# Performance work log

Measured on AMD Instinct MI355X. Metric: run time of the kernel, lower is better.

## Reference

```python
import jax, jax.numpy as jnp
import numpy as np

T, B, D = 512, 64, 1024


def setup_inputs() -> dict:
    key = jax.random.key(0)
    k1, k2, k3, k4 = jax.random.split(key, 4)
    scale = 1.0 / np.sqrt(D)
    x = jax.random.normal(k1, (T, B, D), dtype=jnp.float32)
    resets = jax.random.randint(k2, (T, B), 0, 2) > 0  # bool reset mask per step
    Wi = jax.random.normal(k3, (D, 3 * D), dtype=jnp.float32) * scale  # [ir|iz|in]
    bi = jnp.zeros((3 * D,), dtype=jnp.float32)
    Wh = jax.random.normal(k4, (D, 3 * D), dtype=jnp.float32) * scale  # [hr|hz|hn]
    bhn = jnp.zeros((D,), dtype=jnp.float32)  # bias only on hn gate (flax GRUCell)
    return {"x": x, "Wi": Wi, "bi": bi, "Wh": Wh, "bhn": bhn, "resets": resets}


def reference(x, Wi, bi, Wh, bhn, resets):
    """Scan of flax nn.GRUCell with reset-masked carry. x: [T,B,D], resets: [T,B] bool."""
    Bsz, Dh = x.shape[1], x.shape[2]

    def step(h, inp):
        xt, rt = inp  # xt: [B,D], rt: [B]
        h = jnp.where(rt[:, None], jnp.zeros_like(h), h)  # reset carry to zeros
        gi = xt @ Wi + bi          # [B,3D]
        gh = h @ Wh                # [B,3D] (no bias for r,z in flax GRUCell)
        ir_, iz_, in_ = jnp.split(gi, 3, axis=-1)
        hr_, hz_, hn_ = jnp.split(gh, 3, axis=-1)
        r = jax.nn.sigmoid(ir_ + hr_)
        z = jax.nn.sigmoid(iz_ + hz_)
        n = jnp.tanh(in_ + r * (hn_ + bhn))
        h_new = (1.0 - z) * n + z * h
        return h_new, h_new

    h0 = jnp.zeros((Bsz, Dh), dtype=x.dtype)  # flax initialize_carry default: zeros
    _, ys = jax.lax.scan(step, h0, (x, resets))
    return ys  # [T,B,D]
```

## Files before the change

kernel.cpp:

```cpp
#include <hip/hip_runtime.h>


typedef __attribute__((ext_vector_type(8))) short short8;
typedef __attribute__((ext_vector_type(4))) float f32x4;
typedef __attribute__((ext_vector_type(4))) unsigned int u32x4;

#define DEV static __device__ __forceinline__

constexpr int TT = 512, BB = 64, DD = 1024, TD = 3072;

constexpr size_t WS_FLAGS = 256;
constexpr size_t WS_H = 8192;
constexpr size_t HPLANE = (size_t)BB * DD * 2;
constexpr size_t WS_NEED = WS_H + 4 * HPLANE;

DEV unsigned short f2bf(float f) {
    unsigned u = __builtin_bit_cast(unsigned, f);
    u += 0x7FFFu + ((u >> 16) & 1u);
    return (unsigned short)(u >> 16);
}
DEV float bf2f(unsigned short s) { return __builtin_bit_cast(float, ((unsigned)s) << 16); }

DEV void ld16c(u32x4& r, const unsigned* p) {
    asm volatile("global_load_dwordx4 %0, %1, off sc0 sc1" : "=v"(r) : "v"(p));
}
DEV void ld16(u32x4& r, const unsigned* p) {
    asm volatile("global_load_dwordx4 %0, %1, off" : "=v"(r) : "v"(p));
}
DEV void ld8u(unsigned& r, const unsigned char* p) {
    asm volatile("global_load_ubyte %0, %1, off" : "=v"(r) : "v"(p));
}
DEV void vm0() {
    asm volatile("s_waitcnt vmcnt(0)" ::: "memory");
    __builtin_amdgcn_sched_barrier(0);
}
#define WAITN(n) do { asm volatile("s_waitcnt vmcnt(" #n ")" ::: "memory"); \
                      __builtin_amdgcn_sched_barrier(0); } while (0)

__global__ void pack_x_kernel(const float* __restrict__ x, unsigned* __restrict__ outw) {
    const size_t gid = (size_t)blockIdx.x * 256 + threadIdx.x;
    const size_t e0 = gid * 8;
    const unsigned t = (unsigned)(e0 >> 16);
    const unsigned p = (unsigned)(e0 & 65535u);
    const unsigned r = p >> 10, d = p & 1023u;
    const unsigned m = r >> 4, lr = r & 15u;
    f32x4 a = *(const f32x4*)(x + e0);
    f32x4 b = *(const f32x4*)(x + e0 + 4);
    u32x4 wh, wl;
#pragma unroll
    for (int j = 0; j < 2; ++j) {
        unsigned short h0 = f2bf(a[2 * j]), h1 = f2bf(a[2 * j + 1]);
        wh[j] = (unsigned)h0 | ((unsigned)h1 << 16);
        wl[j] = (unsigned)f2bf(a[2 * j] - bf2f(h0)) | ((unsigned)f2bf(a[2 * j + 1] - bf2f(h1)) << 16);
        unsigned short g0 = f2bf(b[2 * j]), g1 = f2bf(b[2 * j + 1]);
        wh[2 + j] = (unsigned)g0 | ((unsigned)g1 << 16);
        wl[2 + j] = (unsigned)f2bf(b[2 * j] - bf2f(g0)) | ((unsigned)f2bf(b[2 * j + 1] - bf2f(g1)) << 16);
    }
    unsigned* base = outw + (size_t)t * 65536u + m * 16384u + ((lr * 1024u + d) >> 1);
    *(u32x4*)base = wh;
    *(u32x4*)(base + 8192u) = wl;
}

__global__ void prep_kernel(const unsigned char* __restrict__ resets, unsigned char* __restrict__ ws) {
    const int bid = blockIdx.x, tid = threadIdx.x;
    if (bid < 256) {
        ((unsigned*)(ws + WS_H))[bid * 256 + tid] = 0u;
    } else {
        unsigned* w32 = (unsigned*)ws;
        for (int i = tid; i < 2048; i += 256) w32[i] = 0u;
        __shared__ int ca, cb, cc;
        if (tid == 0) { ca = 0; cb = 0; cc = 0; }
        __syncthreads();
        int la = 0, lb = 0, lc = 0;
        for (int o = tid * 16; o < tid * 16 + 16; ++o) {
            unsigned char v = resets[o];
            if (v) {
                if ((o & 3) == 0) la = 1; else lb = 1;
                if ((o & 7) == 4) lc = 1;
            }
        }
        if (la) atomicOr(&ca, 1);
        if (lb) atomicOr(&cb, 1);
        if (lc) atomicOr(&cc, 1);
        __syncthreads();
        if (tid == 0) {
            unsigned stride, boff = 0;
            if (ca && cb)       { stride = 1; }
            else if (!ca && cb) { stride = 4; boff = 3; }
            else if (ca && cc)  { stride = 4; }
            else if (ca)        { stride = 8; }
            else                { stride = 4; }
            w32[0] = stride; w32[1] = boff;
        }
    }
}

__launch_bounds__(512, 1)
__global__ void gru_kernel(const float* __restrict__ Wi, const float* __restrict__ bi,
                           const float* __restrict__ Wh, const float* __restrict__ bhn,
                           const unsigned char* __restrict__ resets,
                           float* __restrict__ out, unsigned char* __restrict__ ws) {
    const int tid = threadIdx.x;
    const int wg = blockIdx.x;
    const int lane = tid & 63;
    const int kw = tid >> 6;
    const int mgrp = wg >> 6;
    const int cg = wg & 63;
    const int c0 = cg * 16;

    unsigned* fl = (unsigned*)(ws + WS_FLAGS) + mgrp * 256;
    const unsigned rstride = ((const unsigned*)ws)[0];
    const unsigned rboff   = ((const unsigned*)ws)[1];

    unsigned short* h_hi[2] = {(unsigned short*)(ws + WS_H),
                               (unsigned short*)(ws + WS_H + 2 * HPLANE)};
    unsigned short* h_lo[2] = {(unsigned short*)(ws + WS_H + HPLANE),
                               (unsigned short*)(ws + WS_H + 3 * HPLANE)};
    unsigned* outw = (unsigned*)out;

    const int lrow = lane & 15;
    const int lk = (lane >> 4) * 8;

    short8 bih[3][4], bhh[3][4], bhl[3][4];
#pragma unroll
    for (int nt = 0; nt < 3; ++nt) {
        const int col = nt * DD + c0 + lrow;
#pragma unroll
        for (int kt = 0; kt < 4; ++kt) {
            const int kb = kw * 128 + kt * 32 + lk;
            short8 a, c, d;
#pragma unroll
            for (int j = 0; j < 8; ++j) {
                float wi = Wi[(size_t)(kb + j) * TD + col];
                a[j] = (short)f2bf(wi);
                float wh = Wh[(size_t)(kb + j) * TD + col];
                unsigned short h2 = f2bf(wh);
                c[j] = (short)h2;
                d[j] = (short)f2bf(wh - bf2f(h2));
            }
            bih[nt][kt] = a; bhh[nt][kt] = c; bhl[nt][kt] = d;
        }
    }

    const int eb = (tid & 255) >> 4, ej = tid & 15;
    const int brow = mgrp * 16 + eb;
    const int ce = c0 + ej;
    const float bi_r = bi[ce], bi_z = bi[DD + ce], bi_n = bi[2 * DD + ce];
    const float bh_n = bhn[ce];
    float h_local = 0.f;
    float ys_prev = 0.f;

    const unsigned xlidx = (unsigned)(lrow * 1024 + kw * 128 + lk);
    const unsigned xwbase = (unsigned)mgrp * 16384u + (xlidx >> 1);
    const unsigned hidx = (unsigned)((mgrp * 16 + lrow) * 1024 + kw * 128 + lk);
    const size_t r64 = (size_t)64 * rstride;
    const size_t roffb = (size_t)brow * rstride + rboff;

    __shared__ float pgi[8][3][16][17];
    __shared__ float pgh[8][3][16][17];
    const int prow = (lane >> 4) * 4;

    {
        const unsigned* xpl = outw;
        u32x4 xf[8];
#pragma unroll
        for (int kt = 0; kt < 4; ++kt) {
            ld16(xf[2 * kt],     xpl + xwbase + kt * 16);
            ld16(xf[2 * kt + 1], xpl + xwbase + 8192u + kt * 16);
        }
        vm0();
        f32x4 ai[3] = {f32x4{0}, f32x4{0}, f32x4{0}};
#pragma unroll
        for (int kt = 0; kt < 4; ++kt) {
            short8 xh = __builtin_bit_cast(short8, xf[2 * kt]);
            short8 xl = __builtin_bit_cast(short8, xf[2 * kt + 1]);
#pragma unroll
            for (int nt = 0; nt < 3; ++nt)
                ai[nt] = __builtin_amdgcn_mfma_f32_16x16x32_bf16(xh, bih[nt][kt], ai[nt], 0, 0, 0);
#pragma unroll
            for (int nt = 0; nt < 3; ++nt)
                ai[nt] = __builtin_amdgcn_mfma_f32_16x16x32_bf16(xl, bih[nt][kt], ai[nt], 0, 0, 0);
        }
#pragma unroll
        for (int s = 0; s < 3; ++s)
#pragma unroll
            for (int i = 0; i < 4; ++i)
                pgi[kw][s][lrow][prow + i] = ai[s][i];
        __syncthreads();
        if (kw < 4 && lane == 0)
            __hip_atomic_store(&fl[cg * 4 + kw], 1u, __ATOMIC_RELAXED, __HIP_MEMORY_SCOPE_AGENT);
    }

    for (int t = 0; t < TT; ++t) {
        {
            const unsigned tgt = (unsigned)(t + 1);
            int guard = 1 << 20;
            while (true) {
                unsigned f0 = __hip_atomic_load(&fl[lane * 4 + 0], __ATOMIC_RELAXED, __HIP_MEMORY_SCOPE_AGENT);
                unsigned f1 = __hip_atomic_load(&fl[lane * 4 + 1], __ATOMIC_RELAXED, __HIP_MEMORY_SCOPE_AGENT);
                unsigned f2 = __hip_atomic_load(&fl[lane * 4 + 2], __ATOMIC_RELAXED, __HIP_MEMORY_SCOPE_AGENT);
                unsigned f3 = __hip_atomic_load(&fl[lane * 4 + 3], __ATOMIC_RELAXED, __HIP_MEMORY_SCOPE_AGENT);
                int ok = (f0 >= tgt) & (f1 >= tgt) & (f2 >= tgt) & (f3 >= tgt);
                if (__all(ok) || --guard == 0) break;
            }
        }
        __builtin_amdgcn_sched_barrier(0);

        const int tn = (t + 1 < TT) ? (t + 1) : (TT - 1);

        unsigned rsv;
        ld8u(rsv, resets + roffb + (size_t)tn * r64);

        const int cur = t & 1;
        const unsigned* hhp = (const unsigned*)h_hi[cur];
        const unsigned* hlp = (const unsigned*)h_lo[cur];
        u32x4 hf[8];
#pragma unroll
        for (int kt = 0; kt < 4; ++kt) {
            ld16c(hf[2 * kt],     hhp + ((hidx + kt * 32) >> 1));
            ld16c(hf[2 * kt + 1], hlp + ((hidx + kt * 32) >> 1));
        }
        const unsigned* xpl = outw + (size_t)tn * 65536u;
        u32x4 xf[8];
#pragma unroll
        for (int kt = 0; kt < 4; ++kt) {
            ld16(xf[2 * kt],     xpl + xwbase + kt * 16);
            ld16(xf[2 * kt + 1], xpl + xwbase + 8192u + kt * 16);
        }

        float g0 = 0.f, g1 = 0.f, g2 = 0.f;
        if (tid < 256) {
#pragma unroll
            for (int k = 0; k < 8; ++k) {
                g0 += pgi[k][0][ej][eb];
                g1 += pgi[k][1][ej][eb];
                g2 += pgi[k][2][ej][eb];
            }
        }

        f32x4 ag[3] = {f32x4{0}, f32x4{0}, f32x4{0}};
        __builtin_amdgcn_s_setprio(1);
        {
            WAITN(14);
            short8 hh = __builtin_bit_cast(short8, hf[0]);
            short8 hl = __builtin_bit_cast(short8, hf[1]);
#pragma unroll
            for (int nt = 0; nt < 3; ++nt) {
                ag[nt] = __builtin_amdgcn_mfma_f32_16x16x32_bf16(hh, bhh[nt][0], ag[nt], 0, 0, 0);
                ag[nt] = __builtin_amdgcn_mfma_f32_16x16x32_bf16(hl, bhh[nt][0], ag[nt], 0, 0, 0);
                ag[nt] = __builtin_amdgcn_mfma_f32_16x16x32_bf16(hh, bhl[nt][0], ag[nt], 0, 0, 0);
            }
        }
        {
            WAITN(12);
            short8 hh = __builtin_bit_cast(short8, hf[2]);
            short8 hl = __builtin_bit_cast(short8, hf[3]);
#pragma unroll
            for (int nt = 0; nt < 3; ++nt) {
                ag[nt] = __builtin_amdgcn_mfma_f32_16x16x32_bf16(hh, bhh[nt][1], ag[nt], 0, 0, 0);
                ag[nt] = __builtin_amdgcn_mfma_f32_16x16x32_bf16(hl, bhh[nt][1], ag[nt], 0, 0, 0);
                ag[nt] = __builtin_amdgcn_mfma_f32_16x16x32_bf16(hh, bhl[nt][1], ag[nt], 0, 0, 0);
            }
        }
        {
            WAITN(10);
            short8 hh = __builtin_bit_cast(short8, hf[4]);
            short8 hl = __builtin_bit_cast(short8, hf[5]);
#pragma unroll
            for (int nt = 0; nt < 3; ++nt) {
                ag[nt] = __builtin_amdgcn_mfma_f32_16x16x32_bf16(hh, bhh[nt][2], ag[nt], 0, 0, 0);
                ag[nt] = __builtin_amdgcn_mfma_f32_16x16x32_bf16(hl, bhh[nt][2], ag[nt], 0, 0, 0);
                ag[nt] = __builtin_amdgcn_mfma_f32_16x16x32_bf16(hh, bhl[nt][2], ag[nt], 0, 0, 0);
            }
        }
        {
            WAITN(8);
            short8 hh = __builtin_bit_cast(short8, hf[6]);
            short8 hl = __builtin_bit_cast(short8, hf[7]);
#pragma unroll
            for (int nt = 0; nt < 3; ++nt) {
                ag[nt] = __builtin_amdgcn_mfma_f32_16x16x32_bf16(hh, bhh[nt][3], ag[nt], 0, 0, 0);
                ag[nt] = __builtin_amdgcn_mfma_f32_16x16x32_bf16(hl, bhh[nt][3], ag[nt], 0, 0, 0);
                ag[nt] = __builtin_amdgcn_mfma_f32_16x16x32_bf16(hh, bhl[nt][3], ag[nt], 0, 0, 0);
            }
        }
        __builtin_amdgcn_s_setprio(0);

#pragma unroll
        for (int s = 0; s < 3; ++s)
#pragma unroll
            for (int i = 0; i < 4; ++i)
                pgh[kw][s][lrow][prow + i] = ag[s][i];
        __syncthreads();

        if (tid < 256) {
            float h0 = 0.f, h1 = 0.f, h2 = 0.f;
#pragma unroll
            for (int k = 0; k < 8; ++k) {
                h0 += pgh[k][0][ej][eb];
                h1 += pgh[k][1][ej][eb];
                h2 += pgh[k][2][ej][eb];
            }
            float r = 1.f / (1.f + __expf(-(g0 + bi_r + h0)));
            float z = 1.f / (1.f + __expf(-(g1 + bi_z + h1)));
            float pre = g2 + bi_n + r * (h2 + bh_n);
            float e2 = __expf(2.f * pre);
            float n = 1.f - 2.f / (e2 + 1.f);
            float hnew = (1.f - z) * n + z * h_local;

            if (t) out[(size_t)(t - 1) * 65536u + brow * DD + ce] = ys_prev;
            ys_prev = hnew;

            if (t < TT - 1) {
                float heff = (rsv != 0u) ? 0.f : hnew;
                h_local = heff;
                unsigned short ph = f2bf(heff);
                unsigned short pl = f2bf(heff - bf2f(ph));
                __hip_atomic_store(h_hi[cur ^ 1] + brow * DD + ce, ph,
                                   __ATOMIC_RELAXED, __HIP_MEMORY_SCOPE_AGENT);
                __hip_atomic_store(h_lo[cur ^ 1] + brow * DD + ce, pl,
                                   __ATOMIC_RELAXED, __HIP_MEMORY_SCOPE_AGENT);
            }
        }

        if (kw < 4) {
            vm0();
            if (lane == 0 && t < TT - 1)
                __hip_atomic_store(&fl[cg * 4 + kw], (unsigned)(t + 2),
                                   __ATOMIC_RELAXED, __HIP_MEMORY_SCOPE_AGENT);
        }

        if (t < TT - 1) {
            WAITN(0);
            f32x4 ai[3] = {f32x4{0}, f32x4{0}, f32x4{0}};
#pragma unroll
            for (int kt = 0; kt < 4; ++kt) {
                short8 xh = __builtin_bit_cast(short8, xf[2 * kt]);
                short8 xl = __builtin_bit_cast(short8, xf[2 * kt + 1]);
#pragma unroll
                for (int nt = 0; nt < 3; ++nt)
                    ai[nt] = __builtin_amdgcn_mfma_f32_16x16x32_bf16(xh, bih[nt][kt], ai[nt], 0, 0, 0);
#pragma unroll
                for (int nt = 0; nt < 3; ++nt)
                    ai[nt] = __builtin_amdgcn_mfma_f32_16x16x32_bf16(xl, bih[nt][kt], ai[nt], 0, 0, 0);
            }
#pragma unroll
            for (int s = 0; s < 3; ++s)
#pragma unroll
                for (int i = 0; i < 4; ++i)
                    pgi[kw][s][lrow][prow + i] = ai[s][i];
            __syncthreads();
        }
    }

    if (tid < 256)
        out[(size_t)(TT - 1) * 65536u + brow * DD + ce] = ys_prev;
}

extern "C" void kernel_launch(void* const* d_in, const int* in_sizes, int n_in,
                              void* d_out, int out_size, void* d_ws, size_t ws_size,
                              hipStream_t stream) {
    const float* x = (const float*)d_in[0];
    const float* Wi = (const float*)d_in[1];
    const float* bi = (const float*)d_in[2];
    const float* Wh = (const float*)d_in[3];
    const float* bhn = (const float*)d_in[4];
    const unsigned char* resets = (const unsigned char*)d_in[5];
    float* out = (float*)d_out;
    unsigned char* ws = (unsigned char*)d_ws;

    if (ws_size < WS_NEED) return;

    hipLaunchKernelGGL(pack_x_kernel, dim3(16384), dim3(256), 0, stream, x, (unsigned*)out);
    hipLaunchKernelGGL(prep_kernel, dim3(257), dim3(256), 0, stream, resets, ws);

    void* args[] = {(void*)&Wi, (void*)&bi, (void*)&Wh, (void*)&bhn,
                    (void*)&resets, (void*)&out, (void*)&ws};
    hipError_t err = hipLaunchCooperativeKernel((const void*)gru_kernel, dim3(256), dim3(512),
                                                args, 0, stream);
    if (err != hipSuccess) {
        hipLaunchKernelGGL(gru_kernel, dim3(256), dim3(512), 0, stream,
                           Wi, bi, Wh, bhn, resets, out, ws);
    }
}
```

Baseline: 3.048 ms.

## Replace per-step flag barrier with tagged hidden-state words for dataflow sync

The separate per-workgroup flag array and its spin-wait are removed. Each hidden-state element is now stored as a 32-bit word with the bf16 value in the high half and a step tag in the low half. Consumers poll the hidden-state data itself until every tag matches the current step, then unpack the halves for the MFMAs. This removes the vmcnt(0) drain and flag store on the producer side, and the extra flag round-trip on the critical path. In exchange it doubles hidden-state traffic, adds unpacking ALU work, and loses the staggered partial waits on the h loads.

```diff
diff --git a/kernel.cpp b/kernel.cpp
--- a/kernel.cpp
+++ b/kernel.cpp
@@ -9,10 +9,9 @@
 
 constexpr int TT = 512, BB = 64, DD = 1024, TD = 3072;
 
-constexpr size_t WS_FLAGS = 256;
 constexpr size_t WS_H = 8192;
-constexpr size_t HPLANE = (size_t)BB * DD * 2;
-constexpr size_t WS_NEED = WS_H + 4 * HPLANE;
+constexpr size_t HP_BYTES = (size_t)BB * DD * 4;
+constexpr size_t WS_NEED = WS_H + 4 * HP_BYTES;
 
 DEV unsigned short f2bf(float f) {
     unsigned u = __builtin_bit_cast(unsigned, f);
@@ -34,8 +33,6 @@
     asm volatile("s_waitcnt vmcnt(0)" ::: "memory");
     __builtin_amdgcn_sched_barrier(0);
 }
-#define WAITN(n) do { asm volatile("s_waitcnt vmcnt(" #n ")" ::: "memory"); \
-                      __builtin_amdgcn_sched_barrier(0); } while (0)
 
 __global__ void pack_x_kernel(const float* __restrict__ x, unsigned* __restrict__ outw) {
     const size_t gid = (size_t)blockIdx.x * 256 + threadIdx.x;
@@ -63,7 +60,7 @@
 
 __global__ void prep_kernel(const unsigned char* __restrict__ resets, unsigned char* __restrict__ ws) {
     const int bid = blockIdx.x, tid = threadIdx.x;
-    if (bid < 256) {
+    if (bid < 512) {
         ((unsigned*)(ws + WS_H))[bid * 256 + tid] = 0u;
     } else {
         unsigned* w32 = (unsigned*)ws;
@@ -108,14 +105,13 @@
     const int cg = wg & 63;
     const int c0 = cg * 16;
 
-    unsigned* fl = (unsigned*)(ws + WS_FLAGS) + mgrp * 256;
     const unsigned rstride = ((const unsigned*)ws)[0];
     const unsigned rboff   = ((const unsigned*)ws)[1];
 
-    unsigned short* h_hi[2] = {(unsigned short*)(ws + WS_H),
-                               (unsigned short*)(ws + WS_H + 2 * HPLANE)};
-    unsigned short* h_lo[2] = {(unsigned short*)(ws + WS_H + HPLANE),
-                               (unsigned short*)(ws + WS_H + 3 * HPLANE)};
+    unsigned* h_hi[2] = {(unsigned*)(ws + WS_H),
+                         (unsigned*)(ws + WS_H + 2 * HP_BYTES)};
+    unsigned* h_lo[2] = {(unsigned*)(ws + WS_H + HP_BYTES),
+                         (unsigned*)(ws + WS_H + 3 * HP_BYTES)};
     unsigned* outw = (unsigned*)out;
 
     const int lrow = lane & 15;
@@ -187,45 +183,45 @@
             for (int i = 0; i < 4; ++i)
                 pgi[kw][s][lrow][prow + i] = ai[s][i];
         __syncthreads();
-        if (kw < 4 && lane == 0)
-            __hip_atomic_store(&fl[cg * 4 + kw], 1u, __ATOMIC_RELAXED, __HIP_MEMORY_SCOPE_AGENT);
     }
 
     for (int t = 0; t < TT; ++t) {
+        const int tn = (t + 1 < TT) ? (t + 1) : (TT - 1);
+
+        unsigned rsv;
+        ld8u(rsv, resets + roffb + (size_t)tn * r64);
+        const unsigned* xpl = outw + (size_t)tn * 65536u;
+        u32x4 xf[8];
+#pragma unroll
+        for (int kt = 0; kt < 4; ++kt) {
+            ld16(xf[2 * kt],     xpl + xwbase + kt * 16);
+            ld16(xf[2 * kt + 1], xpl + xwbase + 8192u + kt * 16);
+        }
+
+        const int cur = t & 1;
+        const unsigned* hip_ = h_hi[cur] + hidx;
+        const unsigned* hlp_ = h_lo[cur] + hidx;
+        const unsigned tag = (unsigned)t & 0xFFFFu;
+        u32x4 ph[8], pl[8];
         {
-            const unsigned tgt = (unsigned)(t + 1);
             int guard = 1 << 20;
             while (true) {
-                unsigned f0 = __hip_atomic_load(&fl[lane * 4 + 0], __ATOMIC_RELAXED, __HIP_MEMORY_SCOPE_AGENT);
-                unsigned f1 = __hip_atomic_load(&fl[lane * 4 + 1], __ATOMIC_RELAXED, __HIP_MEMORY_SCOPE_AGENT);
-                unsigned f2 = __hip_atomic_load(&fl[lane * 4 + 2], __ATOMIC_RELAXED, __HIP_MEMORY_SCOPE_AGENT);
-                unsigned f3 = __hip_atomic_load(&fl[lane * 4 + 3], __ATOMIC_RELAXED, __HIP_MEMORY_SCOPE_AGENT);
-                int ok = (f0 >= tgt) & (f1 >= tgt) & (f2 >= tgt) & (f3 >= tgt);
-                if (__all(ok) || --guard == 0) break;
-            }
-        }
-        __builtin_amdgcn_sched_barrier(0);
-
-        const int tn = (t + 1 < TT) ? (t + 1) : (TT - 1);
-
-        unsigned rsv;
-        ld8u(rsv, resets + roffb + (size_t)tn * r64);
-
-        const int cur = t & 1;
-        const unsigned* hhp = (const unsigned*)h_hi[cur];
-        const unsigned* hlp = (const unsigned*)h_lo[cur];
-        u32x4 hf[8];
-#pragma unroll
-        for (int kt = 0; kt < 4; ++kt) {
-            ld16c(hf[2 * kt],     hhp + ((hidx + kt * 32) >> 1));
-            ld16c(hf[2 * kt + 1], hlp + ((hidx + kt * 32) >> 1));
-        }
-        const unsigned* xpl = outw + (size_t)tn * 65536u;
-        u32x4 xf[8];
-#pragma unroll
-        for (int kt = 0; kt < 4; ++kt) {
-            ld16(xf[2 * kt],     xpl + xwbase + kt * 16);
-            ld16(xf[2 * kt + 1], xpl + xwbase + 8192u + kt * 16);
+#pragma unroll
+                for (int kt = 0; kt < 4; ++kt) {
+                    ld16c(ph[2 * kt],     hip_ + kt * 32);
+                    ld16c(ph[2 * kt + 1], hip_ + kt * 32 + 4);
+                    ld16c(pl[2 * kt],     hlp_ + kt * 32);
+                    ld16c(pl[2 * kt + 1], hlp_ + kt * 32 + 4);
+                }
+                vm0();
+                unsigned bad = 0;
+#pragma unroll
+                for (int i = 0; i < 8; ++i)
+#pragma unroll
+                    for (int j = 0; j < 4; ++j)
+                        bad |= ((ph[i][j] ^ tag) | (pl[i][j] ^ tag)) & 0xFFFFu;
+                if (__all(bad == 0) || --guard == 0) break;
+            }
         }
 
         float g0 = 0.f, g1 = 0.f, g2 = 0.f;
@@ -240,48 +236,24 @@
 
         f32x4 ag[3] = {f32x4{0}, f32x4{0}, f32x4{0}};
         __builtin_amdgcn_s_setprio(1);
-        {
-            WAITN(14);
-            short8 hh = __builtin_bit_cast(short8, hf[0]);
-            short8 hl = __builtin_bit_cast(short8, hf[1]);
+#pragma unroll
+        for (int kt = 0; kt < 4; ++kt) {
+            u32x4 wh, wl;
+            wh[0] = (ph[2 * kt][0] >> 16)     | (ph[2 * kt][1] & 0xFFFF0000u);
+            wh[1] = (ph[2 * kt][2] >> 16)     | (ph[2 * kt][3] & 0xFFFF0000u);
+            wh[2] = (ph[2 * kt + 1][0] >> 16) | (ph[2 * kt + 1][1] & 0xFFFF0000u);
+            wh[3] = (ph[2 * kt + 1][2] >> 16) | (ph[2 * kt + 1][3] & 0xFFFF0000u);
+            wl[0] = (pl[2 * kt][0] >> 16)     | (pl[2 * kt][1] & 0xFFFF0000u);
+            wl[1] = (pl[2 * kt][2] >> 16)     | (pl[2 * kt][3] & 0xFFFF0000u);
+            wl[2] = (pl[2 * kt + 1][0] >> 16) | (pl[2 * kt + 1][1] & 0xFFFF0000u);
+            wl[3] = (pl[2 * kt + 1][2] >> 16) | (pl[2 * kt + 1][3] & 0xFFFF0000u);
+            short8 hh = __builtin_bit_cast(short8, wh);
+            short8 hl = __builtin_bit_cast(short8, wl);
 #pragma unroll
             for (int nt = 0; nt < 3; ++nt) {
-                ag[nt] = __builtin_amdgcn_mfma_f32_16x16x32_bf16(hh, bhh[nt][0], ag[nt], 0, 0, 0);
-                ag[nt] = __builtin_amdgcn_mfma_f32_16x16x32_bf16(hl, bhh[nt][0], ag[nt], 0, 0, 0);
-                ag[nt] = __builtin_amdgcn_mfma_f32_16x16x32_bf16(hh, bhl[nt][0], ag[nt], 0, 0, 0);
-            }
-        }
-        {
-            WAITN(12);
-            short8 hh = __builtin_bit_cast(short8, hf[2]);
-            short8 hl = __builtin_bit_cast(short8, hf[3]);
-#pragma unroll
-            for (int nt = 0; nt < 3; ++nt) {
-                ag[nt] = __builtin_amdgcn_mfma_f32_16x16x32_bf16(hh, bhh[nt][1], ag[nt], 0, 0, 0);
-                ag[nt] = __builtin_amdgcn_mfma_f32_16x16x32_bf16(hl, bhh[nt][1], ag[nt], 0, 0, 0);
-                ag[nt] = __builtin_amdgcn_mfma_f32_16x16x32_bf16(hh, bhl[nt][1], ag[nt], 0, 0, 0);
-            }
-        }
-        {
-            WAITN(10);
-            short8 hh = __builtin_bit_cast(short8, hf[4]);
-            short8 hl = __builtin_bit_cast(short8, hf[5]);
-#pragma unroll
-            for (int nt = 0; nt < 3; ++nt) {
-                ag[nt] = __builtin_amdgcn_mfma_f32_16x16x32_bf16(hh, bhh[nt][2], ag[nt], 0, 0, 0);
-                ag[nt] = __builtin_amdgcn_mfma_f32_16x16x32_bf16(hl, bhh[nt][2], ag[nt], 0, 0, 0);
-                ag[nt] = __builtin_amdgcn_mfma_f32_16x16x32_bf16(hh, bhl[nt][2], ag[nt], 0, 0, 0);
-            }
-        }
-        {
-            WAITN(8);
-            short8 hh = __builtin_bit_cast(short8, hf[6]);
-            short8 hl = __builtin_bit_cast(short8, hf[7]);
-#pragma unroll
-            for (int nt = 0; nt < 3; ++nt) {
-                ag[nt] = __builtin_amdgcn_mfma_f32_16x16x32_bf16(hh, bhh[nt][3], ag[nt], 0, 0, 0);
-                ag[nt] = __builtin_amdgcn_mfma_f32_16x16x32_bf16(hl, bhh[nt][3], ag[nt], 0, 0, 0);
-                ag[nt] = __builtin_amdgcn_mfma_f32_16x16x32_bf16(hh, bhl[nt][3], ag[nt], 0, 0, 0);
+                ag[nt] = __builtin_amdgcn_mfma_f32_16x16x32_bf16(hh, bhh[nt][kt], ag[nt], 0, 0, 0);
+                ag[nt] = __builtin_amdgcn_mfma_f32_16x16x32_bf16(hl, bhh[nt][kt], ag[nt], 0, 0, 0);
+                ag[nt] = __builtin_amdgcn_mfma_f32_16x16x32_bf16(hh, bhl[nt][kt], ag[nt], 0, 0, 0);
             }
         }
         __builtin_amdgcn_s_setprio(0);
@@ -314,24 +286,19 @@
             if (t < TT - 1) {
                 float heff = (rsv != 0u) ? 0.f : hnew;
                 h_local = heff;
-                unsigned short ph = f2bf(heff);
-                unsigned short pl = f2bf(heff - bf2f(ph));
-                __hip_atomic_store(h_hi[cur ^ 1] + brow * DD + ce, ph,
+                const unsigned ntag = (unsigned)(t + 1) & 0xFFFFu;
+                unsigned short ph16 = f2bf(heff);
+                unsigned short pl16 = f2bf(heff - bf2f(ph16));
+                __hip_atomic_store(h_hi[cur ^ 1] + brow * 1024 + ce,
+                                   ((unsigned)ph16 << 16) | ntag,
                                    __ATOMIC_RELAXED, __HIP_MEMORY_SCOPE_AGENT);
-                __hip_atomic_store(h_lo[cur ^ 1] + brow * DD + ce, pl,
+                __hip_atomic_store(h_lo[cur ^ 1] + brow * 1024 + ce,
+                                   ((unsigned)pl16 << 16) | ntag,
                                    __ATOMIC_RELAXED, __HIP_MEMORY_SCOPE_AGENT);
             }
         }
 
-        if (kw < 4) {
-            vm0();
-            if (lane == 0 && t < TT - 1)
-                __hip_atomic_store(&fl[cg * 4 + kw], (unsigned)(t + 2),
-                                   __ATOMIC_RELAXED, __HIP_MEMORY_SCOPE_AGENT);
-        }
-
         if (t < TT - 1) {
-            WAITN(0);
             f32x4 ai[3] = {f32x4{0}, f32x4{0}, f32x4{0}};
 #pragma unroll
             for (int kt = 0; kt < 4; ++kt) {
@@ -372,7 +339,7 @@
     if (ws_size < WS_NEED) return;
 
     hipLaunchKernelGGL(pack_x_kernel, dim3(16384), dim3(256), 0, stream, x, (unsigned*)out);
-    hipLaunchKernelGGL(prep_kernel, dim3(257), dim3(256), 0, stream, resets, ws);
+    hipLaunchKernelGGL(prep_kernel, dim3(513), dim3(256), 0, stream, resets, ws);
 
     void* args[] = {(void*)&Wi, (void*)&bi, (void*)&Wh, (void*)&bhn,
                     (void*)&resets, (void*)&out, (void*)&ws};
```

Measured after the change: 5.332 ms. 74.9% more time.

## Replace per-wave flag polling with counter barrier and move x-projection into critical step

Applied to the files above, without the earlier changes.

Replaces the 256 per-wave progress flags with eight replicated atomic counters per batch group, incremented once per workgroup, so the spin loop polls eight words instead of 256. The input projection for step t is now computed after the barrier, alongside the recurrent MFMAs, and the prefetch of the next x tile is issued after the barrier signal. This cuts polling traffic and removes one __syncthreads per step. In exchange it adds a block-wide __syncthreads before each signal, uses atomic adds contended by eight workgroups per counter, and places the x MFMAs on the serial critical path between barrier and signal.

```diff
diff --git a/kernel.cpp b/kernel.cpp
--- a/kernel.cpp
+++ b/kernel.cpp
@@ -9,7 +9,7 @@
 
 constexpr int TT = 512, BB = 64, DD = 1024, TD = 3072;
 
-constexpr size_t WS_FLAGS = 256;
+constexpr size_t WS_BAR = 256;
 constexpr size_t WS_H = 8192;
 constexpr size_t HPLANE = (size_t)BB * DD * 2;
 constexpr size_t WS_NEED = WS_H + 4 * HPLANE;
@@ -108,7 +108,8 @@
     const int cg = wg & 63;
     const int c0 = cg * 16;
 
-    unsigned* fl = (unsigned*)(ws + WS_FLAGS) + mgrp * 256;
+    unsigned* bar = (unsigned*)(ws + WS_BAR) + mgrp * 256;
+    unsigned* rep = &bar[(cg & 7) * 32];
     const unsigned rstride = ((const unsigned*)ws)[0];
     const unsigned rboff   = ((const unsigned*)ws)[1];
 
@@ -160,49 +161,29 @@
     __shared__ float pgh[8][3][16][17];
     const int prow = (lane >> 4) * 4;
 
+    u32x4 xf[8];
     {
         const unsigned* xpl = outw;
-        u32x4 xf[8];
 #pragma unroll
         for (int kt = 0; kt < 4; ++kt) {
             ld16(xf[2 * kt],     xpl + xwbase + kt * 16);
             ld16(xf[2 * kt + 1], xpl + xwbase + 8192u + kt * 16);
         }
-        vm0();
-        f32x4 ai[3] = {f32x4{0}, f32x4{0}, f32x4{0}};
-#pragma unroll
-        for (int kt = 0; kt < 4; ++kt) {
-            short8 xh = __builtin_bit_cast(short8, xf[2 * kt]);
-            short8 xl = __builtin_bit_cast(short8, xf[2 * kt + 1]);
-#pragma unroll
-            for (int nt = 0; nt < 3; ++nt)
-                ai[nt] = __builtin_amdgcn_mfma_f32_16x16x32_bf16(xh, bih[nt][kt], ai[nt], 0, 0, 0);
-#pragma unroll
-            for (int nt = 0; nt < 3; ++nt)
-                ai[nt] = __builtin_amdgcn_mfma_f32_16x16x32_bf16(xl, bih[nt][kt], ai[nt], 0, 0, 0);
-        }
-#pragma unroll
-        for (int s = 0; s < 3; ++s)
-#pragma unroll
-            for (int i = 0; i < 4; ++i)
-                pgi[kw][s][lrow][prow + i] = ai[s][i];
-        __syncthreads();
-        if (kw < 4 && lane == 0)
-            __hip_atomic_store(&fl[cg * 4 + kw], 1u, __ATOMIC_RELAXED, __HIP_MEMORY_SCOPE_AGENT);
+        if (tid == 0)
+            __hip_atomic_fetch_add(rep, 1u, __ATOMIC_RELAXED, __HIP_MEMORY_SCOPE_AGENT);
     }
 
     for (int t = 0; t < TT; ++t) {
         {
-            const unsigned tgt = (unsigned)(t + 1);
+            const unsigned target = 64u * (unsigned)(t + 1);
             int guard = 1 << 20;
-            while (true) {
-                unsigned f0 = __hip_atomic_load(&fl[lane * 4 + 0], __ATOMIC_RELAXED, __HIP_MEMORY_SCOPE_AGENT);
-                unsigned f1 = __hip_atomic_load(&fl[lane * 4 + 1], __ATOMIC_RELAXED, __HIP_MEMORY_SCOPE_AGENT);
-                unsigned f2 = __hip_atomic_load(&fl[lane * 4 + 2], __ATOMIC_RELAXED, __HIP_MEMORY_SCOPE_AGENT);
-                unsigned f3 = __hip_atomic_load(&fl[lane * 4 + 3], __ATOMIC_RELAXED, __HIP_MEMORY_SCOPE_AGENT);
-                int ok = (f0 >= tgt) & (f1 >= tgt) & (f2 >= tgt) & (f3 >= tgt);
-                if (__all(ok) || --guard == 0) break;
-            }
+            unsigned s;
+            do {
+                s = 0;
+#pragma unroll
+                for (int r2 = 0; r2 < 8; ++r2)
+                    s += __hip_atomic_load(&bar[r2 * 32], __ATOMIC_RELAXED, __HIP_MEMORY_SCOPE_AGENT);
+            } while (s < target && --guard);
         }
         __builtin_amdgcn_sched_barrier(0);
 
@@ -210,7 +191,6 @@
 
         unsigned rsv;
         ld8u(rsv, resets + roffb + (size_t)tn * r64);
-
         const int cur = t & 1;
         const unsigned* hhp = (const unsigned*)h_hi[cur];
         const unsigned* hlp = (const unsigned*)h_lo[cur];
@@ -220,83 +200,85 @@
             ld16c(hf[2 * kt],     hhp + ((hidx + kt * 32) >> 1));
             ld16c(hf[2 * kt + 1], hlp + ((hidx + kt * 32) >> 1));
         }
-        const unsigned* xpl = outw + (size_t)tn * 65536u;
-        u32x4 xf[8];
+
+        WAITN(9);
+        f32x4 ai[3] = {f32x4{0}, f32x4{0}, f32x4{0}};
 #pragma unroll
         for (int kt = 0; kt < 4; ++kt) {
-            ld16(xf[2 * kt],     xpl + xwbase + kt * 16);
-            ld16(xf[2 * kt + 1], xpl + xwbase + 8192u + kt * 16);
-        }
-
-        float g0 = 0.f, g1 = 0.f, g2 = 0.f;
+            short8 xh = __builtin_bit_cast(short8, xf[2 * kt]);
+            short8 xl = __builtin_bit_cast(short8, xf[2 * kt + 1]);
+#pragma unroll
+            for (int nt = 0; nt < 3; ++nt)
+                ai[nt] = __builtin_amdgcn_mfma_f32_16x16x32_bf16(xh, bih[nt][kt], ai[nt], 0, 0, 0);
+#pragma unroll
+            for (int nt = 0; nt < 3; ++nt)
+                ai[nt] = __builtin_amdgcn_mfma_f32_16x16x32_bf16(xl, bih[nt][kt], ai[nt], 0, 0, 0);
+        }
+
+        f32x4 ag[3] = {f32x4{0}, f32x4{0}, f32x4{0}};
+        __builtin_amdgcn_s_setprio(1);
+        {
+            WAITN(6);
+            short8 hh = __builtin_bit_cast(short8, hf[0]);
+            short8 hl = __builtin_bit_cast(short8, hf[1]);
+#pragma unroll
+            for (int nt = 0; nt < 3; ++nt) {
+                ag[nt] = __builtin_amdgcn_mfma_f32_16x16x32_bf16(hh, bhh[nt][0], ag[nt], 0, 0, 0);
+                ag[nt] = __builtin_amdgcn_mfma_f32_16x16x32_bf16(hl, bhh[nt][0], ag[nt], 0, 0, 0);
+                ag[nt] = __builtin_amdgcn_mfma_f32_16x16x32_bf16(hh, bhl[nt][0], ag[nt], 0, 0, 0);
+            }
+        }
+        {
+            WAITN(4);
+            short8 hh = __builtin_bit_cast(short8, hf[2]);
+            short8 hl = __builtin_bit_cast(short8, hf[3]);
+#pragma unroll
+            for (int nt = 0; nt < 3; ++nt) {
+                ag[nt] = __builtin_amdgcn_mfma_f32_16x16x32_bf16(hh, bhh[nt][1], ag[nt], 0, 0, 0);
+                ag[nt] = __builtin_amdgcn_mfma_f32_16x16x32_bf16(hl, bhh[nt][1], ag[nt], 0, 0, 0);
+                ag[nt] = __builtin_amdgcn_mfma_f32_16x16x32_bf16(hh, bhl[nt][1], ag[nt], 0, 0, 0);
+            }
+        }
+        {
+            WAITN(2);
+            short8 hh = __builtin_bit_cast(short8, hf[4]);
+            short8 hl = __builtin_bit_cast(short8, hf[5]);
+#pragma unroll
+            for (int nt = 0; nt < 3; ++nt) {
+                ag[nt] = __builtin_amdgcn_mfma_f32_16x16x32_bf16(hh, bhh[nt][2], ag[nt], 0, 0, 0);
+                ag[nt] = __builtin_amdgcn_mfma_f32_16x16x32_bf16(hl, bhh[nt][2], ag[nt], 0, 0, 0);
+                ag[nt] = __builtin_amdgcn_mfma_f32_16x16x32_bf16(hh, bhl[nt][2], ag[nt], 0, 0, 0);
+            }
+        }
+        {
+            WAITN(0);
+            short8 hh = __builtin_bit_cast(short8, hf[6]);
+            short8 hl = __builtin_bit_cast(short8, hf[7]);
+#pragma unroll
+            for (int nt = 0; nt < 3; ++nt) {
+                ag[nt] = __builtin_amdgcn_mfma_f32_16x16x32_bf16(hh, bhh[nt][3], ag[nt], 0, 0, 0);
+                ag[nt] = __builtin_amdgcn_mfma_f32_16x16x32_bf16(hl, bhh[nt][3], ag[nt], 0, 0, 0);
+                ag[nt] = __builtin_amdgcn_mfma_f32_16x16x32_bf16(hh, bhl[nt][3], ag[nt], 0, 0, 0);
+            }
+        }
+        __builtin_amdgcn_s_setprio(0);
+
+#pragma unroll
+        for (int s = 0; s < 3; ++s)
+#pragma unroll
+            for (int i = 0; i < 4; ++i) {
+                pgi[kw][s][lrow][prow + i] = ai[s][i];
+                pgh[kw][s][lrow][prow + i] = ag[s][i];
+            }
+        __syncthreads();
+
         if (tid < 256) {
+            float g0 = 0.f, g1 = 0.f, g2 = 0.f, h0 = 0.f, h1 = 0.f, h2 = 0.f;
 #pragma unroll
             for (int k = 0; k < 8; ++k) {
                 g0 += pgi[k][0][ej][eb];
                 g1 += pgi[k][1][ej][eb];
                 g2 += pgi[k][2][ej][eb];
-            }
-        }
-
-        f32x4 ag[3] = {f32x4{0}, f32x4{0}, f32x4{0}};
-        __builtin_amdgcn_s_setprio(1);
-        {
-            WAITN(14);
-            short8 hh = __builtin_bit_cast(short8, hf[0]);
-            short8 hl = __builtin_bit_cast(short8, hf[1]);
-#pragma unroll
-            for (int nt = 0; nt < 3; ++nt) {
-                ag[nt] = __builtin_amdgcn_mfma_f32_16x16x32_bf16(hh, bhh[nt][0], ag[nt], 0, 0, 0);
-                ag[nt] = __builtin_amdgcn_mfma_f32_16x16x32_bf16(hl, bhh[nt][0], ag[nt], 0, 0, 0);
-                ag[nt] = __builtin_amdgcn_mfma_f32_16x16x32_bf16(hh, bhl[nt][0], ag[nt], 0, 0, 0);
-            }
-        }
-        {
-            WAITN(12);
-            short8 hh = __builtin_bit_cast(short8, hf[2]);
-            short8 hl = __builtin_bit_cast(short8, hf[3]);
-#pragma unroll
-            for (int nt = 0; nt < 3; ++nt) {
-                ag[nt] = __builtin_amdgcn_mfma_f32_16x16x32_bf16(hh, bhh[nt][1], ag[nt], 0, 0, 0);
-                ag[nt] = __builtin_amdgcn_mfma_f32_16x16x32_bf16(hl, bhh[nt][1], ag[nt], 0, 0, 0);
-                ag[nt] = __builtin_amdgcn_mfma_f32_16x16x32_bf16(hh, bhl[nt][1], ag[nt], 0, 0, 0);
-            }
-        }
-        {
-            WAITN(10);
-            short8 hh = __builtin_bit_cast(short8, hf[4]);
-            short8 hl = __builtin_bit_cast(short8, hf[5]);
-#pragma unroll
-            for (int nt = 0; nt < 3; ++nt) {
-                ag[nt] = __builtin_amdgcn_mfma_f32_16x16x32_bf16(hh, bhh[nt][2], ag[nt], 0, 0, 0);
-                ag[nt] = __builtin_amdgcn_mfma_f32_16x16x32_bf16(hl, bhh[nt][2], ag[nt], 0, 0, 0);
-                ag[nt] = __builtin_amdgcn_mfma_f32_16x16x32_bf16(hh, bhl[nt][2], ag[nt], 0, 0, 0);
-            }
-        }
-        {
-            WAITN(8);
-            short8 hh = __builtin_bit_cast(short8, hf[6]);
-            short8 hl = __builtin_bit_cast(short8, hf[7]);
-#pragma unroll
-            for (int nt = 0; nt < 3; ++nt) {
-                ag[nt] = __builtin_amdgcn_mfma_f32_16x16x32_bf16(hh, bhh[nt][3], ag[nt], 0, 0, 0);
-                ag[nt] = __builtin_amdgcn_mfma_f32_16x16x32_bf16(hl, bhh[nt][3], ag[nt], 0, 0, 0);
-                ag[nt] = __builtin_amdgcn_mfma_f32_16x16x32_bf16(hh, bhl[nt][3], ag[nt], 0, 0, 0);
-            }
-        }
-        __builtin_amdgcn_s_setprio(0);
-
-#pragma unroll
-        for (int s = 0; s < 3; ++s)
-#pragma unroll
-            for (int i = 0; i < 4; ++i)
-                pgh[kw][s][lrow][prow + i] = ag[s][i];
-        __syncthreads();
-
-        if (tid < 256) {
-            float h0 = 0.f, h1 = 0.f, h2 = 0.f;
-#pragma unroll
-            for (int k = 0; k < 8; ++k) {
                 h0 += pgh[k][0][ej][eb];
                 h1 += pgh[k][1][ej][eb];
                 h2 += pgh[k][2][ej][eb];
@@ -323,33 +305,18 @@
             }
         }
 
-        if (kw < 4) {
-            vm0();
-            if (lane == 0 && t < TT - 1)
-                __hip_atomic_store(&fl[cg * 4 + kw], (unsigned)(t + 2),
-                                   __ATOMIC_RELAXED, __HIP_MEMORY_SCOPE_AGENT);
-        }
+        if (kw < 4) vm0();
+        __syncthreads();
+        if (tid == 0 && t < TT - 1)
+            __hip_atomic_fetch_add(rep, 1u, __ATOMIC_RELAXED, __HIP_MEMORY_SCOPE_AGENT);
 
         if (t < TT - 1) {
-            WAITN(0);
-            f32x4 ai[3] = {f32x4{0}, f32x4{0}, f32x4{0}};
+            const unsigned* xpl = outw + (size_t)(t + 1) * 65536u;
 #pragma unroll
             for (int kt = 0; kt < 4; ++kt) {
-                short8 xh = __builtin_bit_cast(short8, xf[2 * kt]);
-                short8 xl = __builtin_bit_cast(short8, xf[2 * kt + 1]);
-#pragma unroll
-                for (int nt = 0; nt < 3; ++nt)
-                    ai[nt] = __builtin_amdgcn_mfma_f32_16x16x32_bf16(xh, bih[nt][kt], ai[nt], 0, 0, 0);
-#pragma unroll
-                for (int nt = 0; nt < 3; ++nt)
-                    ai[nt] = __builtin_amdgcn_mfma_f32_16x16x32_bf16(xl, bih[nt][kt], ai[nt], 0, 0, 0);
-            }
-#pragma unroll
-            for (int s = 0; s < 3; ++s)
-#pragma unroll
-                for (int i = 0; i < 4; ++i)
-                    pgi[kw][s][lrow][prow + i] = ai[s][i];
-            __syncthreads();
+                ld16(xf[2 * kt],     xpl + xwbase + kt * 16);
+                ld16(xf[2 * kt + 1], xpl + xwbase + 8192u + kt * 16);
+            }
         }
     }
 
```

Result: slower. 3.284 ms (+7.7%).
